# Optimization experiments

Measured on AMD Instinct MI355X. Metric: run time of the kernel, lower is better.

The kernel has to match this reference:

```python
import jax, jax.numpy as jnp
import numpy as np

NUM_IN, NUM_OUT, SD, BATCH = 2048, 8192, 5, 4096
INIT_DELTA = 0.01


def _dist(a, b):
    # a: [I,1,D], b: [1,O,D] -> [I,O]
    return jnp.sqrt(jnp.sum((a - b) ** 2, axis=-1))


def setup_inputs() -> dict:
    key = jax.random.key(0)
    k1, k2, k3, k4, k5 = jax.random.split(key, 5)
    init_in_pos = jax.random.normal(k1, (NUM_IN, 1, SD), dtype=jnp.float32)
    init_out_pos = jax.random.normal(k2, (1, NUM_OUT, SD), dtype=jnp.float32)
    in_pos = init_in_pos + INIT_DELTA * jax.random.normal(k3, (NUM_IN, 1, SD), dtype=jnp.float32)
    out_pos = init_out_pos + INIT_DELTA * jax.random.normal(k4, (1, NUM_OUT, SD), dtype=jnp.float32)
    inputs = jax.random.normal(k5, (BATCH, NUM_IN), dtype=jnp.float32)
    biases = jnp.zeros((NUM_OUT,), dtype=jnp.float32)
    return {"inputs": inputs, "init_in_pos": init_in_pos, "init_out_pos": init_out_pos,
            "in_pos": in_pos, "out_pos": out_pos, "biases": biases}


def reference(inputs, init_in_pos, init_out_pos, in_pos, out_pos, biases):
    # weight = ||in_pos - out_pos|| - ||init_in_pos - init_out_pos||, shape [I,O]
    w = _dist(in_pos, out_pos) - _dist(init_in_pos, init_out_pos)
    return inputs @ w + biases
```

## Files before the change

kernel.cpp:

```cpp
#include <hip/hip_runtime.h>
#include <hip/hip_bf16.h>
#include <stdint.h>

#define NUM_IN  2048
#define NUM_OUT 8192
#define BATCH   4096
#define SD      5

#define BM 256
#define BN 256
#define BK 64
#define NT (NUM_IN / BK)
#define TILEE (BM * BK)

typedef __bf16 bf16x8 __attribute__((ext_vector_type(8)));
typedef float  f32x4  __attribute__((ext_vector_type(4)));
typedef unsigned short ushort_t;
typedef ushort_t ushort8 __attribute__((ext_vector_type(8)));

static __device__ __forceinline__ ushort_t bf16_bits(float f) {
  __hip_bfloat16 h = __float2bfloat16(f);
  ushort_t u;
  __builtin_memcpy(&u, &h, 2);
  return u;
}

__global__ __launch_bounds__(256) void aux_kernel(
    const float* __restrict__ inputs,
    ushort_t* __restrict__ Abf,
    const float* __restrict__ in_pos, const float* __restrict__ out_pos,
    const float* __restrict__ init_in, const float* __restrict__ init_out,
    ushort_t* __restrict__ Wt) {
  __shared__ float s_ip[NUM_IN * SD];
  __shared__ float s_iip[NUM_IN * SD];
  const int tid = threadIdx.x;

  if (blockIdx.x >= 512) {
    const size_t base = (size_t)(blockIdx.x - 512) * 16384;
#pragma unroll
    for (int c = 0; c < 8; ++c) {
      const size_t i = base + (size_t)c * 2048 + tid * 8;
      float4 v0 = *reinterpret_cast<const float4*>(inputs + i);
      float4 v1 = *reinterpret_cast<const float4*>(inputs + i + 4);
      ushort8 o;
      o[0] = bf16_bits(v0.x); o[1] = bf16_bits(v0.y);
      o[2] = bf16_bits(v0.z); o[3] = bf16_bits(v0.w);
      o[4] = bf16_bits(v1.x); o[5] = bf16_bits(v1.y);
      o[6] = bf16_bits(v1.z); o[7] = bf16_bits(v1.w);
      *reinterpret_cast<ushort8*>(Abf + i) = o;
    }
    return;
  }

#pragma unroll
  for (int i = 0; i < 10; ++i) {
    const int idx = i * 1024 + tid * 4;
    *reinterpret_cast<float4*>(&s_ip[idx]) =
        *reinterpret_cast<const float4*>(in_pos + idx);
    *reinterpret_cast<float4*>(&s_iip[idx]) =
        *reinterpret_cast<const float4*>(init_in + idx);
  }
  __syncthreads();

  const int n  = blockIdx.x * 16 + (tid >> 4);
  const int kg = tid & 15;
  float op[SD], iop[SD];
#pragma unroll
  for (int d = 0; d < SD; ++d) {
    op[d]  = out_pos[n * SD + d];
    iop[d] = init_out[n * SD + d];
  }
#pragma unroll 1
  for (int kb = 0; kb < 16; ++kb) {
    const int k0 = kb * 128 + kg * 8;
    float buf[40], ibuf[40];
#pragma unroll
    for (int j = 0; j < 10; ++j) {
      float4 v = *reinterpret_cast<const float4*>(&s_ip[k0 * SD + j * 4]);
      buf[4 * j + 0] = v.x; buf[4 * j + 1] = v.y;
      buf[4 * j + 2] = v.z; buf[4 * j + 3] = v.w;
      float4 u = *reinterpret_cast<const float4*>(&s_iip[k0 * SD + j * 4]);
      ibuf[4 * j + 0] = u.x; ibuf[4 * j + 1] = u.y;
      ibuf[4 * j + 2] = u.z; ibuf[4 * j + 3] = u.w;
    }
    ushort8 o;
#pragma unroll
    for (int i = 0; i < 8; ++i) {
      float d1 = 0.f, d0 = 0.f;
#pragma unroll
      for (int d = 0; d < SD; ++d) {
        float a = buf[i * SD + d] - op[d];
        float b = ibuf[i * SD + d] - iop[d];
        d1 += a * a;
        d0 += b * b;
      }
      o[i] = bf16_bits(sqrtf(d1) - sqrtf(d0));
    }
    *reinterpret_cast<ushort8*>(Wt + (size_t)n * NUM_IN + k0) = o;
  }
}

__global__ __launch_bounds__(512, 1) void gemm_kernel(
    const ushort_t* __restrict__ A,
    const ushort_t* __restrict__ Bt,
    const float* __restrict__ bias,
    float* __restrict__ C) {
  __shared__ __align__(16) ushort_t sA[2 * TILEE];
  __shared__ __align__(16) ushort_t sB[2 * TILEE];

  const int tid  = threadIdx.x;
  const int w    = tid >> 6;
  const int l    = tid & 63;
  const int wm   = w >> 2;
  const int wn   = w & 3;
  const int lrow = l & 15;
  const int lkc  = l >> 4;

  const int orig = blockIdx.x;
  const int lin  = (orig & 7) * 64 + (orig >> 3);
  const int bx   = lin >> 4;
  const int by   = lin & 15;
  const int m0   = by * BM;
  const int n0   = bx * BN;

  const int ck0 = (lkc ^ (lrow & 7)) * 8;
  const int ck1 = ((4 + lkc) ^ (lrow & 7)) * 8;
  const int Ab  = wm * 4096 + lrow * 64;
  const int Bb  = wn * 2048 + lrow * 64;

  const int d0 = tid, d1 = tid + 512;
  const int lr0 = d0 >> 3, lr1 = d1 >> 3;
  const int c0 = (d0 & 7) ^ (lr0 & 7);
  const int c1 = (d1 & 7) ^ (lr1 & 7);
  const ushort_t* pA0 = A  + (size_t)(m0 + (lr0 >> 6) * 128 + (lr0 & 63)) * NUM_IN + c0 * 8;
  const ushort_t* pA1 = A  + (size_t)(m0 + (lr1 >> 6) * 128 + (lr1 & 63)) * NUM_IN + c1 * 8;
  const ushort_t* pB0 = Bt + (size_t)(n0 + (lr0 >> 5) * 64 + (lr0 & 31)) * NUM_IN + c0 * 8;
  const ushort_t* pB1 = Bt + (size_t)(n0 + (lr1 >> 5) * 64 + (lr1 & 31)) * NUM_IN + c1 * 8;

#define GLDS(src, dst)                                                         \
  __builtin_amdgcn_global_load_lds(                                            \
      reinterpret_cast<const __attribute__((address_space(1))) uint32_t*>(     \
          (uintptr_t)(src)),                                                   \
      reinterpret_cast<__attribute__((address_space(3))) uint32_t*>(           \
          (uintptr_t)(dst)),                                                   \
      16, 0, 0)

#define STAGE_A(bs, mh, kt)                                                    \
  {                                                                            \
    GLDS(pA0 + (size_t)(mh) * 64 * NUM_IN + (kt),                              \
         &sA[(bs) * TILEE + (mh) * 8192 + tid * 8]);                           \
    GLDS(pA1 + (size_t)(mh) * 64 * NUM_IN + (kt),                              \
         &sA[(bs) * TILEE + (mh) * 8192 + tid * 8 + 4096]);                    \
  }
#define STAGE_B(bs, nh, kt)                                                    \
  {                                                                            \
    GLDS(pB0 + (size_t)(nh) * 32 * NUM_IN + (kt),                              \
         &sB[(bs) * TILEE + (nh) * 8192 + tid * 8]);                           \
    GLDS(pB1 + (size_t)(nh) * 32 * NUM_IN + (kt),                              \
         &sB[(bs) * TILEE + (nh) * 8192 + tid * 8 + 4096]);                    \
  }

#define RD_A(arr, bs, mh, ck)                                                  \
  {                                                                            \
    _Pragma("unroll")                                                          \
    for (int mi = 0; mi < 4; ++mi)                                             \
      arr[mi] = *reinterpret_cast<const bf16x8*>(                              \
          &sA[(bs) * TILEE + (mh) * 8192 + Ab + mi * 1024 + (ck)]);            \
  }
#define RD_B(arr, bs, nh, ck)                                                  \
  {                                                                            \
    _Pragma("unroll")                                                          \
    for (int nj = 0; nj < 2; ++nj)                                             \
      arr[nj] = *reinterpret_cast<const bf16x8*>(                              \
          &sB[(bs) * TILEE + (nh) * 8192 + Bb + nj * 1024 + (ck)]);            \
  }

#define MFMA8(mh, nh, Aa, Bb_)                                                 \
  {                                                                            \
    __builtin_amdgcn_s_setprio(1);                                             \
    _Pragma("unroll")                                                          \
    for (int mi = 0; mi < 4; ++mi)                                             \
      _Pragma("unroll")                                                        \
      for (int nj = 0; nj < 2; ++nj)                                           \
        acc[(mh) * 4 + mi][(nh) * 2 + nj] =                                    \
            __builtin_amdgcn_mfma_f32_16x16x32_bf16(                           \
                Aa[mi], Bb_[nj], acc[(mh) * 4 + mi][(nh) * 2 + nj], 0, 0, 0);  \
    __builtin_amdgcn_s_setprio(0);                                             \
  }

#define LGKM(n)  asm volatile("s_waitcnt lgkmcnt(" #n ")" ::: "memory")
#define SCHED0   __builtin_amdgcn_sched_barrier(0)
#define BARRIER  __builtin_amdgcn_s_barrier()
#define VMCNT0   asm volatile("s_waitcnt vmcnt(0)" ::: "memory")

#define KTILE(CUR, NXT, ktn)                                                   \
  {                                                                            \
    STAGE_A(NXT, 0, ktn)                                                       \
    RD_A(aE, CUR, 0, ck0) RD_B(b0, CUR, 0, ck0)                                \
    RD_B(b1, CUR, 1, ck0)                                    \
    LGKM(2); SCHED0;                                                           \
    MFMA8(0, 0, aE, b0)                                                        \
    STAGE_B(NXT, 0, ktn)                                                       \
    RD_A(aO, CUR, 1, ck0)                                    \
    LGKM(4); SCHED0;                                                           \
    MFMA8(0, 1, aE, b1)                                                        \
    STAGE_A(NXT, 1, ktn)                                                       \
    LGKM(0); SCHED0;                                                           \
    MFMA8(1, 0, aO, b0)                                                        \
    STAGE_B(NXT, 1, ktn)                                                       \
    RD_A(aE, CUR, 0, ck1) RD_B(b0, CUR, 0, ck1)              \
    MFMA8(1, 1, aO, b1)                                                        \
    RD_B(b1, CUR, 1, ck1)                                    \
    LGKM(2); SCHED0;                                                           \
    MFMA8(0, 0, aE, b0)                                                        \
    RD_A(aO, CUR, 1, ck1)                                    \
    LGKM(4); SCHED0;                                                           \
    MFMA8(0, 1, aE, b1)                                                        \
    LGKM(0); SCHED0;                                                           \
    MFMA8(1, 0, aO, b0)                                                        \
    MFMA8(1, 1, aO, b1)                                                        \
    VMCNT0;                                                                    \
    BARRIER;                                                                   \
  }

  f32x4 acc[8][4];
#pragma unroll
  for (int i = 0; i < 8; ++i)
#pragma unroll
    for (int j = 0; j < 4; ++j) acc[i][j] = f32x4{0.f, 0.f, 0.f, 0.f};

  bf16x8 aE[4], aO[4], b0[2], b1[2];

  STAGE_A(0, 0, 0) STAGE_B(0, 0, 0) STAGE_A(0, 1, 0) STAGE_B(0, 1, 0)
  VMCNT0;
  BARRIER;

#pragma unroll 1
  for (int tt = 0; tt < NT; tt += 2) {
    const int k1 = (tt + 1) * BK;
    const int k2 = (tt + 2 < NT ? tt + 2 : NT - 1) * BK;
    KTILE(0, 1, k1)
    KTILE(1, 0, k2)
  }

  const int er = l >> 4;
  const int ec = l & 15;
#pragma unroll
  for (int nh = 0; nh < 2; ++nh) {
#pragma unroll
    for (int nj = 0; nj < 2; ++nj) {
      const int col = n0 + wn * 64 + nh * 32 + nj * 16 + ec;
      const float bi = bias[col];
#pragma unroll
      for (int mh = 0; mh < 2; ++mh) {
#pragma unroll
        for (int mi = 0; mi < 4; ++mi) {
#pragma unroll
          for (int j = 0; j < 4; ++j) {
            const int row = m0 + wm * 128 + mh * 64 + mi * 16 + er * 4 + j;
            C[(size_t)row * NUM_OUT + col] =
                acc[mh * 4 + mi][nh * 2 + nj][j] + bi;
          }
        }
      }
    }
  }
#undef KTILE
#undef STAGE_A
#undef STAGE_B
#undef RD_A
#undef RD_B
#undef MFMA8
#undef GLDS
}

extern "C" void kernel_launch(void* const* d_in, const int* in_sizes, int n_in,
                              void* d_out, int out_size, void* d_ws, size_t ws_size,
                              hipStream_t stream) {
  const float* inputs   = (const float*)d_in[0];
  const float* init_in  = (const float*)d_in[1];
  const float* init_out = (const float*)d_in[2];
  const float* in_pos   = (const float*)d_in[3];
  const float* out_pos  = (const float*)d_in[4];
  const float* biases   = (const float*)d_in[5];
  float* out = (float*)d_out;

  ushort_t* Abf = (ushort_t*)d_ws;
  ushort_t* Wt  = (ushort_t*)((char*)d_ws + (size_t)BATCH * NUM_IN * 2);

  aux_kernel<<<1024, 256, 0, stream>>>(inputs, Abf,
                                       in_pos, out_pos, init_in, init_out, Wt);
  gemm_kernel<<<(BATCH / BM) * (NUM_OUT / BN), 512, 0, stream>>>(
      Abf, Wt, biases, out);
}
```

Before: 152.9 us.

## Switch GEMM inner loop from 16x16x32 to 32x32x16 bf16 MFMA

Replaces the 16x16x32 MFMA tiling with 32x32x16 MFMA instructions. Each wave now holds a 4x2 grid of 32x32 accumulator blocks, and the LDS read addressing, swizzled k-chunk offsets, interleaving schedule and epilogue store mapping are rewritten to match. The larger MFMA shape reduces LDS fragment reads per flop and the number of MFMA issues. In exchange the scheduling pattern and waitcnt placement change, and the epilogue store layout differs.

```diff
diff --git a/kernel.cpp b/kernel.cpp
--- a/kernel.cpp
+++ b/kernel.cpp
@@ -14,7 +14,7 @@
 #define TILEE (BM * BK)
 
 typedef __bf16 bf16x8 __attribute__((ext_vector_type(8)));
-typedef float  f32x4  __attribute__((ext_vector_type(4)));
+typedef float  f32x16 __attribute__((ext_vector_type(16)));
 typedef unsigned short ushort_t;
 typedef ushort_t ushort8 __attribute__((ext_vector_type(8)));
 
@@ -113,8 +113,9 @@
   const int l    = tid & 63;
   const int wm   = w >> 2;
   const int wn   = w & 3;
-  const int lrow = l & 15;
-  const int lkc  = l >> 4;
+  const int rl   = l & 31;
+  const int hi   = l >> 5;
+  const int swz  = l & 7;
 
   const int orig = blockIdx.x;
   const int lin  = (orig & 7) * 64 + (orig >> 3);
@@ -123,10 +124,12 @@
   const int m0   = by * BM;
   const int n0   = bx * BN;
 
-  const int ck0 = (lkc ^ (lrow & 7)) * 8;
-  const int ck1 = ((4 + lkc) ^ (lrow & 7)) * 8;
-  const int Ab  = wm * 4096 + lrow * 64;
-  const int Bb  = wn * 2048 + lrow * 64;
+  const int cks0 = ((0 + hi) ^ swz) * 8;
+  const int cks1 = ((2 + hi) ^ swz) * 8;
+  const int cks2 = ((4 + hi) ^ swz) * 8;
+  const int cks3 = ((6 + hi) ^ swz) * 8;
+  const int AbW = (wm * 64 + rl) * 64;
+  const int BbW = (wn * 32 + rl) * 64;
 
   const int d0 = tid, d1 = tid + 512;
   const int lr0 = d0 >> 3, lr1 = d1 >> 3;
@@ -160,31 +163,30 @@
          &sB[(bs) * TILEE + (nh) * 8192 + tid * 8 + 4096]);                    \
   }
 
-#define RD_A(arr, bs, mh, ck)                                                  \
+#define RD_A32(arr, bs, ck)                                                    \
   {                                                                            \
     _Pragma("unroll")                                                          \
-    for (int mi = 0; mi < 4; ++mi)                                             \
-      arr[mi] = *reinterpret_cast<const bf16x8*>(                              \
-          &sA[(bs) * TILEE + (mh) * 8192 + Ab + mi * 1024 + (ck)]);            \
-  }
-#define RD_B(arr, bs, nh, ck)                                                  \
+    for (int mb = 0; mb < 4; ++mb)                                             \
+      arr[mb] = *reinterpret_cast<const bf16x8*>(                              \
+          &sA[(bs) * TILEE + (mb >> 1) * 8192 + (mb & 1) * 2048 + AbW + (ck)]);\
+  }
+#define RD_B32(arr, bs, ck)                                                    \
   {                                                                            \
     _Pragma("unroll")                                                          \
-    for (int nj = 0; nj < 2; ++nj)                                             \
-      arr[nj] = *reinterpret_cast<const bf16x8*>(                              \
-          &sB[(bs) * TILEE + (nh) * 8192 + Bb + nj * 1024 + (ck)]);            \
-  }
-
-#define MFMA8(mh, nh, Aa, Bb_)                                                 \
+    for (int nb = 0; nb < 2; ++nb)                                             \
+      arr[nb] = *reinterpret_cast<const bf16x8*>(                              \
+          &sB[(bs) * TILEE + nb * 8192 + BbW + (ck)]);                         \
+  }
+
+#define MFMA8(Aa, Bx)                                                          \
   {                                                                            \
     __builtin_amdgcn_s_setprio(1);                                             \
     _Pragma("unroll")                                                          \
-    for (int mi = 0; mi < 4; ++mi)                                             \
+    for (int mb = 0; mb < 4; ++mb)                                             \
       _Pragma("unroll")                                                        \
-      for (int nj = 0; nj < 2; ++nj)                                           \
-        acc[(mh) * 4 + mi][(nh) * 2 + nj] =                                    \
-            __builtin_amdgcn_mfma_f32_16x16x32_bf16(                           \
-                Aa[mi], Bb_[nj], acc[(mh) * 4 + mi][(nh) * 2 + nj], 0, 0, 0);  \
+      for (int nb = 0; nb < 2; ++nb)                                           \
+        acc[mb][nb] = __builtin_amdgcn_mfma_f32_32x32x16_bf16(                 \
+            Aa[mb], Bx[nb], acc[mb][nb], 0, 0, 0);                             \
     __builtin_amdgcn_s_setprio(0);                                             \
   }
 
@@ -196,40 +198,34 @@
 #define KTILE(CUR, NXT, ktn)                                                   \
   {                                                                            \
     STAGE_A(NXT, 0, ktn)                                                       \
-    RD_A(aE, CUR, 0, ck0) RD_B(b0, CUR, 0, ck0)                                \
-    RD_B(b1, CUR, 1, ck0)                                    \
-    LGKM(2); SCHED0;                                                           \
-    MFMA8(0, 0, aE, b0)                                                        \
+    RD_A32(aX, CUR, cks0) RD_B32(bX, CUR, cks0)                                \
+    RD_A32(aY, CUR, cks1) RD_B32(bY, CUR, cks1)                                \
+    LGKM(6); SCHED0;                                                           \
+    MFMA8(aX, bX)                                                              \
     STAGE_B(NXT, 0, ktn)                                                       \
-    RD_A(aO, CUR, 1, ck0)                                    \
-    LGKM(4); SCHED0;                                                           \
-    MFMA8(0, 1, aE, b1)                                                        \
+    RD_A32(aX, CUR, cks2) RD_B32(bX, CUR, cks2)                                \
+    LGKM(6); SCHED0;                                                           \
+    MFMA8(aY, bY)                                                              \
     STAGE_A(NXT, 1, ktn)                                                       \
+    RD_A32(aY, CUR, cks3) RD_B32(bY, CUR, cks3)                                \
+    LGKM(6); SCHED0;                                                           \
+    MFMA8(aX, bX)                                                              \
+    STAGE_B(NXT, 1, ktn)                                                       \
     LGKM(0); SCHED0;                                                           \
-    MFMA8(1, 0, aO, b0)                                                        \
-    STAGE_B(NXT, 1, ktn)                                                       \
-    RD_A(aE, CUR, 0, ck1) RD_B(b0, CUR, 0, ck1)              \
-    MFMA8(1, 1, aO, b1)                                                        \
-    RD_B(b1, CUR, 1, ck1)                                    \
-    LGKM(2); SCHED0;                                                           \
-    MFMA8(0, 0, aE, b0)                                                        \
-    RD_A(aO, CUR, 1, ck1)                                    \
-    LGKM(4); SCHED0;                                                           \
-    MFMA8(0, 1, aE, b1)                                                        \
-    LGKM(0); SCHED0;                                                           \
-    MFMA8(1, 0, aO, b0)                                                        \
-    MFMA8(1, 1, aO, b1)                                                        \
+    MFMA8(aY, bY)                                                              \
     VMCNT0;                                                                    \
     BARRIER;                                                                   \
   }
 
-  f32x4 acc[8][4];
-#pragma unroll
-  for (int i = 0; i < 8; ++i)
-#pragma unroll
-    for (int j = 0; j < 4; ++j) acc[i][j] = f32x4{0.f, 0.f, 0.f, 0.f};
-
-  bf16x8 aE[4], aO[4], b0[2], b1[2];
+  f32x16 acc[4][2];
+#pragma unroll
+  for (int i = 0; i < 4; ++i)
+#pragma unroll
+    for (int j = 0; j < 2; ++j)
+#pragma unroll
+      for (int r = 0; r < 16; ++r) acc[i][j][r] = 0.f;
+
+  bf16x8 aX[4], aY[4], bX[2], bY[2];
 
   STAGE_A(0, 0, 0) STAGE_B(0, 0, 0) STAGE_A(0, 1, 0) STAGE_B(0, 1, 0)
   VMCNT0;
@@ -243,33 +239,25 @@
     KTILE(1, 0, k2)
   }
 
-  const int er = l >> 4;
-  const int ec = l & 15;
-#pragma unroll
-  for (int nh = 0; nh < 2; ++nh) {
-#pragma unroll
-    for (int nj = 0; nj < 2; ++nj) {
-      const int col = n0 + wn * 64 + nh * 32 + nj * 16 + ec;
-      const float bi = bias[col];
-#pragma unroll
-      for (int mh = 0; mh < 2; ++mh) {
-#pragma unroll
-        for (int mi = 0; mi < 4; ++mi) {
-#pragma unroll
-          for (int j = 0; j < 4; ++j) {
-            const int row = m0 + wm * 128 + mh * 64 + mi * 16 + er * 4 + j;
-            C[(size_t)row * NUM_OUT + col] =
-                acc[mh * 4 + mi][nh * 2 + nj][j] + bi;
-          }
-        }
+  const int crow = m0 + wm * 128 + 4 * hi;
+  const int ccol = n0 + wn * 64 + rl;
+#pragma unroll
+  for (int nb = 0; nb < 2; ++nb) {
+    const float bi = bias[ccol + nb * 32];
+#pragma unroll
+    for (int mb = 0; mb < 4; ++mb) {
+#pragma unroll
+      for (int reg = 0; reg < 16; ++reg) {
+        const int r = crow + mb * 32 + (reg & 3) + 8 * (reg >> 2);
+        C[(size_t)r * NUM_OUT + ccol + nb * 32] = acc[mb][nb][reg] + bi;
       }
     }
   }
 #undef KTILE
 #undef STAGE_A
 #undef STAGE_B
-#undef RD_A
-#undef RD_B
+#undef RD_A32
+#undef RD_B32
 #undef MFMA8
 #undef GLDS
 }
```

New measurement: 172.0 us. 1.12x slower.
